# Kernel optimization log

Hardware: AMD Instinct MI355X
Metric: run time of the kernel (lower is better)

The kernel has to match this reference:

```python
import jax, jax.numpy as jnp
import numpy as np

N = 100000      # nodes
E = 1200000     # edges (before self-loops)
DIN = 64        # n_input
DH = 64         # n_hidden
DOUT = 40       # n_output (classes)
L = 2           # n_layers
K = 4           # n_heads
ALPHA = 0.2
EPS = 1e-5


def setup_inputs() -> dict:
    key = jax.random.key(0)
    ks = jax.random.split(key, 12)
    s = lambda k, shape: jax.random.normal(k, shape, jnp.float32) * 0.05
    return {
        "x": jax.random.normal(ks[0], (N, DIN), jnp.float32),
        "edge_index": jax.random.randint(ks[1], (2, E), 0, N),
        # GCNConv weights: per layer l, per head k. conv_h: hidden->hidden, conv_x: input->hidden
        "Wh": s(ks[2], (L, K, DH, DH)), "bh": jnp.zeros((L, K, DH), jnp.float32),
        "Wx": s(ks[3], (L, K, DIN, DH)), "bx": jnp.zeros((L, K, DH), jnp.float32),
        # shared GatedModule
        "gf_w": s(ks[4], (2 * DH, 1)), "gf_b": jnp.zeros((1,), jnp.float32),
        "gu_w": s(ks[5], (2 * DH, 1)), "gu_b": jnp.zeros((1,), jnp.float32),
        # per-block FF
        "ff1_w": s(ks[6], (L, DH, DH)), "ff1_b": jnp.zeros((L, DH), jnp.float32),
        "ff2_w": s(ks[7], (L, DH, DH)), "ff2_b": jnp.zeros((L, DH), jnp.float32),
        # classifier head
        "clf1_w": s(ks[8], (DH, DH)), "clf1_b": jnp.zeros((DH,), jnp.float32),
        "clf2_w": s(ks[9], (DH, DOUT)), "clf2_b": jnp.zeros((DOUT,), jnp.float32),
    }


def _layer_norm(h):
    mu = jnp.mean(h, axis=-1, keepdims=True)
    var = jnp.mean((h - mu) ** 2, axis=-1, keepdims=True)
    return (h - mu) * jax.lax.rsqrt(var + EPS)


def reference(x, edge_index, Wh, bh, Wx, bx, gf_w, gf_b, gu_w, gu_b,
              ff1_w, ff1_b, ff2_w, ff2_b, clf1_w, clf1_b, clf2_w, clf2_b):
    # GCN normalization with self-loops: D^-1/2 (A+I) D^-1/2
    loops = jnp.arange(N)
    src = jnp.concatenate([edge_index[0], loops])  # [E+N]
    dst = jnp.concatenate([edge_index[1], loops])
    deg = jax.ops.segment_sum(jnp.ones_like(src, jnp.float32), dst, num_segments=N)
    dinv = jnp.where(deg > 0, jax.lax.rsqrt(jnp.maximum(deg, 1e-12)), 0.0)
    norm = dinv[src] * dinv[dst]  # [E+N] edge coefficients (shared by all convs)

    def gcn_conv(feat, W, b):
        m = feat @ W                                    # [N, DH] transform first (cheaper)
        agg = jax.ops.segment_sum(m[src] * norm[:, None], dst, num_segments=N)
        return agg + b

    def gate(h, xg):
        g = jnp.concatenate([h, xg], axis=1)            # [N, 2*DH]
        f = ALPHA * jnp.tanh(g @ gf_w + gf_b)
        u = ALPHA * jnp.tanh(g @ gu_w + gu_b)
        return (1.0 + f) * h + (1.0 + u) * xg

    h = jnp.zeros((N, DH), x.dtype)  # h0 = zeros (dropout is identity in eval mode)
    for l in range(L):
        acc = jnp.zeros((N, DH), x.dtype)
        for k in range(K):
            hk = gcn_conv(h, Wh[l, k], bh[l, k])
            xk = gcn_conv(x, Wx[l, k], bx[l, k])
            acc = acc + gate(hk, xk)
        h = acc / K + h                                  # multi-head mean + residual
        h = _layer_norm(h)
        ff = jax.nn.relu(h @ ff1_w[l] + ff1_b[l]) @ ff2_w[l] + ff2_b[l]
        h = _layer_norm(ff + h)
    return jax.nn.relu(h @ clf1_w + clf1_b) @ clf2_w + clf2_b
```

## Files before the change

### kernel.cpp

```cpp
#include <hip/hip_runtime.h>

#define NN 100000
#define EE 1200000
#define ALPHA_C 0.2f
#define EPS_C 1e-5f

typedef __attribute__((ext_vector_type(8))) short short8;
typedef __attribute__((ext_vector_type(4))) float f32x4;
#define MFMA __builtin_amdgcn_mfma_f32_16x16x32_bf16

#define PITCH 72


__device__ __forceinline__ ushort f2bf(float f) {
  unsigned u = __float_as_uint(f);
  unsigned r = (u + 0x7FFFu + ((u >> 16) & 1u)) >> 16;
  return (ushort)r;
}
__device__ __forceinline__ float bf2f(ushort h) { return __uint_as_float((unsigned)h << 16); }

__device__ __forceinline__ float ftanh(float x) {
  float ax = fabsf(x);
  float e = __expf(2.f * ax);
  float t = 1.f - 2.f / (e + 1.f);
  return copysignf(t, x);
}


__global__ __launch_bounds__(256) void k_count(const int* __restrict__ dstv, int* __restrict__ deg) {
  int e = blockIdx.x * 256 + threadIdx.x;
  if (e < EE) atomicAdd(&deg[dstv[e]], 1);
}

__global__ __launch_bounds__(256) void k_scan1(const int* __restrict__ deg, int* __restrict__ rowp,
                                               int* __restrict__ bsum, float* __restrict__ dinv) {
  __shared__ int s[256];
  int t = threadIdx.x;
  int i = blockIdx.x * 256 + t;
  int v = (i < NN) ? deg[i] : 0;
  if (i < NN) dinv[i] = rsqrtf((float)v + 1.0f);
  s[t] = v;
  __syncthreads();
  for (int off = 1; off < 256; off <<= 1) {
    int add = (t >= off) ? s[t - off] : 0;
    __syncthreads();
    s[t] += add;
    __syncthreads();
  }
  if (i < NN) rowp[i] = s[t] - v;
  if (t == 255) bsum[blockIdx.x] = s[255];
}

__global__ __launch_bounds__(512) void k_scan2(int* __restrict__ bsum, int* __restrict__ rowp, int nb) {
  __shared__ int s[512];
  int t = threadIdx.x;
  int v = (t < nb) ? bsum[t] : 0;
  s[t] = v;
  __syncthreads();
  for (int off = 1; off < 512; off <<= 1) {
    int add = (t >= off) ? s[t - off] : 0;
    __syncthreads();
    s[t] += add;
    __syncthreads();
  }
  if (t < nb) bsum[t] = s[t] - v;
  if (t == 0) rowp[NN] = EE;
}

__global__ __launch_bounds__(256) void k_scan3(int* __restrict__ rowp, const int* __restrict__ bsum) {
  int i = blockIdx.x * 256 + threadIdx.x;
  if (i < NN) rowp[i] += bsum[blockIdx.x];
}

__global__ __launch_bounds__(256) void k_fill(const int* __restrict__ srcv, const int* __restrict__ dstv,
                                              const int* __restrict__ rowp, int* __restrict__ fill,
                                              int* __restrict__ col) {
  int e = blockIdx.x * 256 + threadIdx.x;
  if (e < EE) {
    int d = dstv[e];
    int pos = rowp[d] + atomicAdd(&fill[d], 1);
    col[pos] = srcv[e];
  }
}


__global__ __launch_bounds__(256) void k_prescale(const float* __restrict__ feat,
                                                  const float* __restrict__ dinv,
                                                  float* __restrict__ xs) {
  int idx = blockIdx.x * 256 + threadIdx.x;
  if (idx < NN * 16) {
    float4 v = ((const float4*)feat)[idx];
    float d = dinv[idx >> 4];
    v.x *= d; v.y *= d; v.z *= d; v.w *= d;
    ((float4*)xs)[idx] = v;
  }
}

__global__ __launch_bounds__(256) void k_spmm(const float4* __restrict__ xs4, const float* __restrict__ dinv,
                                              const int* __restrict__ rowp, const int* __restrict__ col,
                                              float4* __restrict__ out4) {
  int node = blockIdx.x * 16 + (threadIdx.x >> 4);
  int q = threadIdx.x & 15;
  if (node >= NN) return;
  int s = rowp[node], e = rowp[node + 1];
  float4 a0 = {0.f, 0.f, 0.f, 0.f}, a1 = a0, a2 = a0, a3 = a0;
  int j = s;
  for (; j + 4 <= e; j += 4) {
    int c0 = col[j], c1 = col[j + 1], c2 = col[j + 2], c3 = col[j + 3];
    float4 v0 = xs4[c0 * 16 + q];
    float4 v1 = xs4[c1 * 16 + q];
    float4 v2 = xs4[c2 * 16 + q];
    float4 v3 = xs4[c3 * 16 + q];
    a0 += v0; a1 += v1; a2 += v2; a3 += v3;
  }
  for (; j < e; ++j) a0 += xs4[col[j] * 16 + q];
  float4 sv = xs4[node * 16 + q];
  float d = dinv[node];
  float4 o;
  o.x = d * (a0.x + a1.x + a2.x + a3.x + sv.x);
  o.y = d * (a0.y + a1.y + a2.y + a3.y + sv.y);
  o.z = d * (a0.z + a1.z + a2.z + a3.z + sv.z);
  o.w = d * (a0.w + a1.w + a2.w + a3.w + sv.w);
  out4[node * 16 + q] = o;
}


__global__ __launch_bounds__(256) void k_packz(const float* __restrict__ Wh, const float* __restrict__ Wx,
                                               const float* __restrict__ ff1w, const float* __restrict__ ff2w,
                                               const float* __restrict__ c1w, const float* __restrict__ c2w,
                                               ushort* __restrict__ wpk,
                                               int* __restrict__ deg, int* __restrict__ fill) {
  int i = blockIdx.x * 256 + threadIdx.x;
  if (i < NN) { deg[i] = 0; fill[i] = 0; }
  int id = blockIdx.x;
  if (id >= 22) return;
  const float* src;
  int ncol = 64, vcol = 64;
  if (id < 8) src = Wx + id * 4096;
  else if (id < 16) src = Wh + (id - 8) * 4096;
  else if (id < 18) src = ff1w + (id - 16) * 4096;
  else if (id < 20) src = ff2w + (id - 18) * 4096;
  else if (id == 20) src = c1w;
  else { src = c2w; ncol = 40; vcol = 40; }
  ushort* dst = wpk + (size_t)id * 8192;
  for (int p = threadIdx.x; p < 512; p += 256) {
    int f = p >> 6, l = p & 63;
    int kh = f & 1, tc = f >> 1;
    int r0 = 32 * kh + 8 * (l >> 4), c = 16 * tc + (l & 15);
#pragma unroll
    for (int j = 0; j < 8; ++j) {
      float v = (c < vcol) ? src[(r0 + j) * ncol + c] : 0.f;
      ushort h = f2bf(v);
      dst[f * 512 + l * 8 + j] = h;
      dst[4096 + f * 512 + l * 8 + j] = f2bf(v - bf2f(h));
    }
  }
}


__device__ __forceinline__ float red16(float v) {
  v += __shfl_xor(v, 1);
  v += __shfl_xor(v, 2);
  v += __shfl_xor(v, 4);
  v += __shfl_xor(v, 8);
  return v;
}

__device__ __forceinline__ void stage_tile(const float* __restrict__ src, int gbase,
                                           ushort* __restrict__ hi, ushort* __restrict__ lo, int t) {
#pragma unroll
  for (int u = 0; u < 4; ++u) {
    int f = u * 256 + t;
    int row = f >> 4, c4 = (f & 15) << 2;
    int gr = gbase + row;
    if (gr > NN - 1) gr = NN - 1;
    float4 v = *(const float4*)(src + gr * 64 + c4);
    ushort h0 = f2bf(v.x), h1 = f2bf(v.y), h2 = f2bf(v.z), h3 = f2bf(v.w);
    ushort l0 = f2bf(v.x - bf2f(h0)), l1 = f2bf(v.y - bf2f(h1)),
           l2 = f2bf(v.z - bf2f(h2)), l3 = f2bf(v.w - bf2f(h3));
    int o = row * PITCH + c4;
    *(ushort4*)(hi + o) = make_ushort4(h0, h1, h2, h3);
    *(ushort4*)(lo + o) = make_ushort4(l0, l1, l2, l3);
  }
}

__device__ __forceinline__ void stageB(const ushort* __restrict__ wp, ushort* __restrict__ bsta, int t) {
#pragma unroll
  for (int u = 0; u < 4; ++u) {
    int o = (u * 256 + t) * 8;
    *(short8*)(bsta + o) = *(const short8*)(wp + o);
  }
}

template <int NT>
__device__ __forceinline__ void mm_mfma_l(short8 a0h, short8 a1h, short8 a0l, short8 a1l,
                                          const ushort* __restrict__ bsta, int l, f32x4* C) {
#pragma unroll
  for (int tc = 0; tc < NT; ++tc) {
#pragma unroll
    for (int kh = 0; kh < 2; ++kh) {
      const short8 bh = *(const short8*)(bsta + (tc * 2 + kh) * 512 + l * 8);
      const short8 bl = *(const short8*)(bsta + 4096 + (tc * 2 + kh) * 512 + l * 8);
      const short8 ah = kh ? a1h : a0h;
      const short8 alo = kh ? a1l : a0l;
      C[tc] = MFMA(ah, bh, C[tc], 0, 0, 0);
      C[tc] = MFMA(ah, bl, C[tc], 0, 0, 0);
      C[tc] = MFMA(alo, bh, C[tc], 0, 0, 0);
    }
  }
}

__device__ __forceinline__ void ln_frag(float v[4][4]) {
#pragma unroll
  for (int r = 0; r < 4; ++r) {
    float s = v[0][r] + v[1][r] + v[2][r] + v[3][r];
    s = red16(s);
    float mu = s * 0.015625f;
    float q = 0.f;
#pragma unroll
    for (int tc = 0; tc < 4; ++tc) { float d = v[tc][r] - mu; q = fmaf(d, d, q); }
    q = red16(q);
    float inv = rsqrtf(q * 0.015625f + EPS_C);
#pragma unroll
    for (int tc = 0; tc < 4; ++tc) v[tc][r] = (v[tc][r] - mu) * inv;
  }
}


template <int HAS_H, int WSC, int DO_CLF>
__global__ __launch_bounds__(256) void k_layer(
    const float* __restrict__ aggX, const float* __restrict__ aggH,
    const float* __restrict__ h_in, float* __restrict__ h_out,
    float* __restrict__ hs_out, const float* __restrict__ dinv,
    const ushort* __restrict__ wxp, const ushort* __restrict__ whp,
    const float* __restrict__ bxl, const float* __restrict__ bhl,
    const float* __restrict__ gfw, const float* __restrict__ gfb,
    const float* __restrict__ guw, const float* __restrict__ gub,
    const ushort* __restrict__ ff1p, const float* __restrict__ ff1b,
    const ushort* __restrict__ ff2p, const float* __restrict__ ff2b,
    const ushort* __restrict__ c1p, const float* __restrict__ c1b,
    const ushort* __restrict__ c2p, const float* __restrict__ c2b,
    float* __restrict__ outv) {
  __shared__ __align__(16) ushort th[64 * PITCH], tl[64 * PITCH];
  __shared__ __align__(16) ushort bsta[8192];
  const int t = threadIdx.x, blk = blockIdx.x;
  const int w = t >> 6, l = t & 63, lg = l >> 4, lr = l & 15;
  const int abase = (16 * w + lr) * PITCH + 8 * lg;

  stage_tile(aggX, blk * 64, th, tl, t);
  __syncthreads();
  short8 xa0h = *(const short8*)(th + abase);
  short8 xa1h = *(const short8*)(th + abase + 32);
  short8 xa0l = *(const short8*)(tl + abase);
  short8 xa1l = *(const short8*)(tl + abase + 32);
  short8 ha0h = (short8)0, ha1h = (short8)0, ha0l = (short8)0, ha1l = (short8)0;
  if (HAS_H) {
    __syncthreads();
    stage_tile(aggH, blk * 64, th, tl, t);
    __syncthreads();
    ha0h = *(const short8*)(th + abase);
    ha1h = *(const short8*)(th + abase + 32);
    ha0l = *(const short8*)(tl + abase);
    ha1l = *(const short8*)(tl + abase + 32);
  }

  float gfhw[4], gfxw[4], guhw[4], guxw[4];
#pragma unroll
  for (int tc = 0; tc < 4; ++tc) {
    gfhw[tc] = gfw[lr + 16 * tc]; gfxw[tc] = gfw[64 + lr + 16 * tc];
    guhw[tc] = guw[lr + 16 * tc]; guxw[tc] = guw[64 + lr + 16 * tc];
  }
  const float gfb0 = gfb[0], gub0 = gub[0];

  float acc[4][4];
#pragma unroll
  for (int tc = 0; tc < 4; ++tc)
#pragma unroll
    for (int r = 0; r < 4; ++r) acc[tc][r] = 0.f;

  for (int k = 0; k < 4; ++k) {
    f32x4 cx[4], ch[4];
#pragma unroll
    for (int tc = 0; tc < 4; ++tc) { cx[tc] = (f32x4)0.f; ch[tc] = (f32x4)0.f; }
    __syncthreads();
    stageB(wxp + k * 8192, bsta, t);
    __syncthreads();
    mm_mfma_l<4>(xa0h, xa1h, xa0l, xa1l, bsta, l, cx);
    if (HAS_H) {
      __syncthreads();
      stageB(whp + k * 8192, bsta, t);
      __syncthreads();
      mm_mfma_l<4>(ha0h, ha1h, ha0l, ha1l, bsta, l, ch);
    }

    float Cx[4][4], Ch[4][4];
#pragma unroll
    for (int tc = 0; tc < 4; ++tc) {
      float bxv = bxl[k * 64 + lr + 16 * tc];
      float bhv = bhl[k * 64 + lr + 16 * tc];
#pragma unroll
      for (int r = 0; r < 4; ++r) {
        Cx[tc][r] = cx[tc][r] + bxv;
        Ch[tc][r] = (HAS_H ? ch[tc][r] : 0.f) + bhv;
      }
    }
#pragma unroll
    for (int r = 0; r < 4; ++r) {
      float pf = 0.f, pu = 0.f;
#pragma unroll
      for (int tc = 0; tc < 4; ++tc) {
        pf = fmaf(Ch[tc][r], gfhw[tc], pf); pf = fmaf(Cx[tc][r], gfxw[tc], pf);
        pu = fmaf(Ch[tc][r], guhw[tc], pu); pu = fmaf(Cx[tc][r], guxw[tc], pu);
      }
      pf = red16(pf); pu = red16(pu);
      float fv = ALPHA_C * ftanh(pf + gfb0);
      float uv = ALPHA_C * ftanh(pu + gub0);
#pragma unroll
      for (int tc = 0; tc < 4; ++tc)
        acc[tc][r] += (1.f + fv) * Ch[tc][r] + (1.f + uv) * Cx[tc][r];
    }
  }

  float hmid[4][4];
#pragma unroll
  for (int tc = 0; tc < 4; ++tc)
#pragma unroll
    for (int r = 0; r < 4; ++r) {
      float hv = 0.f;
      if (HAS_H) {
        int gn = blk * 64 + 16 * w + 4 * lg + r;
        if (gn > NN - 1) gn = NN - 1;
        hv = h_in[gn * 64 + lr + 16 * tc];
      }
      hmid[tc][r] = fmaf(acc[tc][r], 0.25f, hv);
    }
  ln_frag(hmid);

  __syncthreads();
#pragma unroll
  for (int tc = 0; tc < 4; ++tc)
#pragma unroll
    for (int r = 0; r < 4; ++r) {
      int o = (16 * w + 4 * lg + r) * PITCH + lr + 16 * tc;
      ushort h = f2bf(hmid[tc][r]);
      th[o] = h;
      tl[o] = f2bf(hmid[tc][r] - bf2f(h));
    }
  __syncthreads();
  short8 m0h = *(const short8*)(th + abase);
  short8 m1h = *(const short8*)(th + abase + 32);
  short8 m0l = *(const short8*)(tl + abase);
  short8 m1l = *(const short8*)(tl + abase + 32);

  f32x4 f1[4];
#pragma unroll
  for (int tc = 0; tc < 4; ++tc) f1[tc] = (f32x4)0.f;
  __syncthreads();
  stageB(ff1p, bsta, t);
  __syncthreads();
  mm_mfma_l<4>(m0h, m1h, m0l, m1l, bsta, l, f1);
#pragma unroll
  for (int tc = 0; tc < 4; ++tc) {
    float bv = ff1b[lr + 16 * tc];
#pragma unroll
    for (int r = 0; r < 4; ++r) {
      float v = fmaxf(f1[tc][r] + bv, 0.f);
      int o = (16 * w + 4 * lg + r) * PITCH + lr + 16 * tc;
      ushort h = f2bf(v);
      th[o] = h;
      tl[o] = f2bf(v - bf2f(h));
    }
  }
  __syncthreads();
  short8 g0h = *(const short8*)(th + abase);
  short8 g1h = *(const short8*)(th + abase + 32);
  short8 g0l = *(const short8*)(tl + abase);
  short8 g1l = *(const short8*)(tl + abase + 32);

  f32x4 f2[4];
#pragma unroll
  for (int tc = 0; tc < 4; ++tc) f2[tc] = (f32x4)0.f;
  __syncthreads();
  stageB(ff2p, bsta, t);
  __syncthreads();
  mm_mfma_l<4>(g0h, g1h, g0l, g1l, bsta, l, f2);
  float F2[4][4];
#pragma unroll
  for (int tc = 0; tc < 4; ++tc) {
    float bv = ff2b[lr + 16 * tc];
#pragma unroll
    for (int r = 0; r < 4; ++r) F2[tc][r] = f2[tc][r] + bv + hmid[tc][r];
  }
  ln_frag(F2);

  if (!DO_CLF) {
#pragma unroll
    for (int r = 0; r < 4; ++r) {
      int gn = blk * 64 + 16 * w + 4 * lg + r;
      if (gn < NN) {
        float dv = WSC ? dinv[gn] : 0.f;
#pragma unroll
        for (int tc = 0; tc < 4; ++tc) {
          h_out[gn * 64 + lr + 16 * tc] = F2[tc][r];
          if (WSC) hs_out[gn * 64 + lr + 16 * tc] = F2[tc][r] * dv;
        }
      }
    }
    return;
  }

  __syncthreads();
#pragma unroll
  for (int tc = 0; tc < 4; ++tc)
#pragma unroll
    for (int r = 0; r < 4; ++r) {
      int o = (16 * w + 4 * lg + r) * PITCH + lr + 16 * tc;
      ushort h = f2bf(F2[tc][r]);
      th[o] = h;
      tl[o] = f2bf(F2[tc][r] - bf2f(h));
    }
  stageB(c1p, bsta, t);
  __syncthreads();
  short8 p0h = *(const short8*)(th + abase);
  short8 p1h = *(const short8*)(th + abase + 32);
  short8 p0l = *(const short8*)(tl + abase);
  short8 p1l = *(const short8*)(tl + abase + 32);

  f32x4 c1[4];
#pragma unroll
  for (int tc = 0; tc < 4; ++tc) c1[tc] = (f32x4)0.f;
  mm_mfma_l<4>(p0h, p1h, p0l, p1l, bsta, l, c1);
  __syncthreads();
#pragma unroll
  for (int tc = 0; tc < 4; ++tc) {
    float bv = c1b[lr + 16 * tc];
#pragma unroll
    for (int r = 0; r < 4; ++r) {
      float v = fmaxf(c1[tc][r] + bv, 0.f);
      int o = (16 * w + 4 * lg + r) * PITCH + lr + 16 * tc;
      ushort hh = f2bf(v);
      th[o] = hh;
      tl[o] = f2bf(v - bf2f(hh));
    }
  }
  stageB(c2p, bsta, t);
  __syncthreads();
  short8 q0h = *(const short8*)(th + abase);
  short8 q1h = *(const short8*)(th + abase + 32);
  short8 q0l = *(const short8*)(tl + abase);
  short8 q1l = *(const short8*)(tl + abase + 32);

  f32x4 c2[3];
#pragma unroll
  for (int tc = 0; tc < 3; ++tc) c2[tc] = (f32x4)0.f;
  mm_mfma_l<3>(q0h, q1h, q0l, q1l, bsta, l, c2);
#pragma unroll
  for (int tc = 0; tc < 3; ++tc) {
    int cc = lr + 16 * tc;
    if (cc < 40) {
      float bv = c2b[cc];
#pragma unroll
      for (int r = 0; r < 4; ++r) {
        int gn = blk * 64 + 16 * w + 4 * lg + r;
        if (gn < NN) outv[gn * 40 + cc] = c2[tc][r] + bv;
      }
    }
  }
}


extern "C" void kernel_launch(void* const* d_in, const int* in_sizes, int n_in,
                              void* d_out, int out_size, void* d_ws, size_t ws_size,
                              hipStream_t stream) {
  (void)in_sizes; (void)n_in; (void)out_size; (void)ws_size;
  const float* x    = (const float*)d_in[0];
  const int*   ei   = (const int*)d_in[1];
  const float* Wh   = (const float*)d_in[2];
  const float* bh   = (const float*)d_in[3];
  const float* Wx   = (const float*)d_in[4];
  const float* bx   = (const float*)d_in[5];
  const float* gfw  = (const float*)d_in[6];
  const float* gfb  = (const float*)d_in[7];
  const float* guw  = (const float*)d_in[8];
  const float* gub  = (const float*)d_in[9];
  const float* ff1w = (const float*)d_in[10];
  const float* ff1b = (const float*)d_in[11];
  const float* ff2w = (const float*)d_in[12];
  const float* ff2b = (const float*)d_in[13];
  const float* c1w  = (const float*)d_in[14];
  const float* c1b  = (const float*)d_in[15];
  const float* c2w  = (const float*)d_in[16];
  const float* c2b  = (const float*)d_in[17];
  float* outv = (float*)d_out;

  char* ws = (char*)d_ws;
  size_t o = 0;
  auto take = [&](size_t b) { char* p = ws + o; o += (b + 255) & ~(size_t)255; return p; };
  int*    deg  = (int*)take((size_t)NN * 4);
  int*    fill = (int*)take((size_t)NN * 4);
  int*    rowp = (int*)take((size_t)(NN + 1) * 4);
  int*    bsum = (int*)take(512 * 4);
  int*    col  = (int*)take((size_t)EE * 4);
  float*  dinv = (float*)take((size_t)NN * 4);
  ushort* wpk  = (ushort*)take((size_t)22 * 8192 * 2);
  float*  aggX = (float*)take((size_t)NN * 64 * 4);
  float*  aggH = (float*)take((size_t)NN * 64 * 4);
  float*  hbuf = (float*)take((size_t)NN * 64 * 4);
  float*  xsc  = (float*)take((size_t)NN * 64 * 4);

  const int* srcv = ei;
  const int* dstv = ei + EE;

  const int NB_E = (EE + 255) / 256;
  const int NB_N = (NN + 255) / 256;
  const int NB_V4 = (NN * 16 + 255) / 256;

  k_packz<<<NB_N, 256, 0, stream>>>(Wh, Wx, ff1w, ff2w, c1w, c2w, wpk, deg, fill);
  k_count<<<NB_E, 256, 0, stream>>>(dstv, deg);
  k_scan1<<<NB_N, 256, 0, stream>>>(deg, rowp, bsum, dinv);
  k_scan2<<<1, 512, 0, stream>>>(bsum, rowp, NB_N);
  k_scan3<<<NB_N, 256, 0, stream>>>(rowp, bsum);
  k_fill<<<NB_E, 256, 0, stream>>>(srcv, dstv, rowp, fill, col);

  k_prescale<<<NB_V4, 256, 0, stream>>>(x, dinv, xsc);
  k_spmm<<<(NN + 15) / 16, 256, 0, stream>>>((const float4*)xsc, dinv, rowp, col, (float4*)aggX);

  const int NB_L = (NN + 63) / 64;
  k_layer<0, 1, 0><<<NB_L, 256, 0, stream>>>(
      aggX, aggX, hbuf, hbuf, xsc, dinv,
      wpk + 0 * 8192, wpk + 8 * 8192, bx, bh, gfw, gfb, guw, gub,
      wpk + 16 * 8192, ff1b, wpk + 18 * 8192, ff2b,
      wpk + 20 * 8192, c1b, wpk + 21 * 8192, c2b, outv);

  k_spmm<<<(NN + 15) / 16, 256, 0, stream>>>((const float4*)xsc, dinv, rowp, col, (float4*)aggH);

  k_layer<1, 0, 1><<<NB_L, 256, 0, stream>>>(
      aggX, aggH, hbuf, hbuf, xsc, dinv,
      wpk + 4 * 8192, wpk + 12 * 8192, bx + 256, bh + 256, gfw, gfb, guw, gub,
      wpk + 17 * 8192, ff1b + 64, wpk + 19 * 8192, ff2b + 64,
      wpk + 20 * 8192, c1b, wpk + 21 * 8192, c2b, outv);
}
```

Measured before the change: 380.9 us.

## Emit bf16 hi/lo split from SpMM and record edge rank during counting

The SpMM kernel now writes its aggregated features directly as packed bf16 hi/lo halves. The layer kernels then load their MFMA A-fragments straight from global memory, with no shared-memory staging, conversion or barriers. Separately, the degree-count kernel stores each edge's atomic rank, so the CSR fill pass no longer needs a second atomic pass or a fill array. The cost is an extra 4.8 MB rank buffer and per-lane strided global loads in place of the LDS tile.

Measured after the change: 338.0 us. 1.13x faster.

```diff
diff --git a/kernel.cpp b/kernel.cpp
--- a/kernel.cpp
+++ b/kernel.cpp
@@ -27,9 +27,10 @@
 }
 
 
-__global__ __launch_bounds__(256) void k_count(const int* __restrict__ dstv, int* __restrict__ deg) {
+__global__ __launch_bounds__(256) void k_countrank(const int* __restrict__ dstv,
+                                                   int* __restrict__ deg, int* __restrict__ rank) {
   int e = blockIdx.x * 256 + threadIdx.x;
-  if (e < EE) atomicAdd(&deg[dstv[e]], 1);
+  if (e < EE) rank[e] = atomicAdd(&deg[dstv[e]], 1);
 }
 
 __global__ __launch_bounds__(256) void k_scan1(const int* __restrict__ deg, int* __restrict__ rowp,
@@ -73,14 +74,10 @@
 }
 
 __global__ __launch_bounds__(256) void k_fill(const int* __restrict__ srcv, const int* __restrict__ dstv,
-                                              const int* __restrict__ rowp, int* __restrict__ fill,
+                                              const int* __restrict__ rowp, const int* __restrict__ rank,
                                               int* __restrict__ col) {
   int e = blockIdx.x * 256 + threadIdx.x;
-  if (e < EE) {
-    int d = dstv[e];
-    int pos = rowp[d] + atomicAdd(&fill[d], 1);
-    col[pos] = srcv[e];
-  }
+  if (e < EE) col[rowp[dstv[e]] + rank[e]] = srcv[e];
 }
 
 
@@ -98,7 +95,7 @@
 
 __global__ __launch_bounds__(256) void k_spmm(const float4* __restrict__ xs4, const float* __restrict__ dinv,
                                               const int* __restrict__ rowp, const int* __restrict__ col,
-                                              float4* __restrict__ out4) {
+                                              ushort* __restrict__ outP) {
   int node = blockIdx.x * 16 + (threadIdx.x >> 4);
   int q = threadIdx.x & 15;
   if (node >= NN) return;
@@ -121,17 +118,21 @@
   o.y = d * (a0.y + a1.y + a2.y + a3.y + sv.y);
   o.z = d * (a0.z + a1.z + a2.z + a3.z + sv.z);
   o.w = d * (a0.w + a1.w + a2.w + a3.w + sv.w);
-  out4[node * 16 + q] = o;
+  ushort h0 = f2bf(o.x), h1 = f2bf(o.y), h2 = f2bf(o.z), h3 = f2bf(o.w);
+  ushort l0 = f2bf(o.x - bf2f(h0)), l1 = f2bf(o.y - bf2f(h1)),
+         l2 = f2bf(o.z - bf2f(h2)), l3 = f2bf(o.w - bf2f(h3));
+  ushort* p = outP + (size_t)node * 128 + 4 * q;
+  *(ushort4*)(p) = make_ushort4(h0, h1, h2, h3);
+  *(ushort4*)(p + 64) = make_ushort4(l0, l1, l2, l3);
 }
 
 
 __global__ __launch_bounds__(256) void k_packz(const float* __restrict__ Wh, const float* __restrict__ Wx,
                                                const float* __restrict__ ff1w, const float* __restrict__ ff2w,
                                                const float* __restrict__ c1w, const float* __restrict__ c2w,
-                                               ushort* __restrict__ wpk,
-                                               int* __restrict__ deg, int* __restrict__ fill) {
+                                               ushort* __restrict__ wpk, int* __restrict__ deg) {
   int i = blockIdx.x * 256 + threadIdx.x;
-  if (i < NN) { deg[i] = 0; fill[i] = 0; }
+  if (i < NN) deg[i] = 0;
   int id = blockIdx.x;
   if (id >= 22) return;
   const float* src;
@@ -166,24 +167,6 @@
   return v;
 }
 
-__device__ __forceinline__ void stage_tile(const float* __restrict__ src, int gbase,
-                                           ushort* __restrict__ hi, ushort* __restrict__ lo, int t) {
-#pragma unroll
-  for (int u = 0; u < 4; ++u) {
-    int f = u * 256 + t;
-    int row = f >> 4, c4 = (f & 15) << 2;
-    int gr = gbase + row;
-    if (gr > NN - 1) gr = NN - 1;
-    float4 v = *(const float4*)(src + gr * 64 + c4);
-    ushort h0 = f2bf(v.x), h1 = f2bf(v.y), h2 = f2bf(v.z), h3 = f2bf(v.w);
-    ushort l0 = f2bf(v.x - bf2f(h0)), l1 = f2bf(v.y - bf2f(h1)),
-           l2 = f2bf(v.z - bf2f(h2)), l3 = f2bf(v.w - bf2f(h3));
-    int o = row * PITCH + c4;
-    *(ushort4*)(hi + o) = make_ushort4(h0, h1, h2, h3);
-    *(ushort4*)(lo + o) = make_ushort4(l0, l1, l2, l3);
-  }
-}
-
 __device__ __forceinline__ void stageB(const ushort* __restrict__ wp, ushort* __restrict__ bsta, int t) {
 #pragma unroll
   for (int u = 0; u < 4; ++u) {
@@ -229,7 +212,7 @@
 
 template <int HAS_H, int WSC, int DO_CLF>
 __global__ __launch_bounds__(256) void k_layer(
-    const float* __restrict__ aggX, const float* __restrict__ aggH,
+    const ushort* __restrict__ aggXP, const ushort* __restrict__ aggHP,
     const float* __restrict__ h_in, float* __restrict__ h_out,
     float* __restrict__ hs_out, const float* __restrict__ dinv,
     const ushort* __restrict__ wxp, const ushort* __restrict__ whp,
@@ -246,22 +229,21 @@
   const int t = threadIdx.x, blk = blockIdx.x;
   const int w = t >> 6, l = t & 63, lg = l >> 4, lr = l & 15;
   const int abase = (16 * w + lr) * PITCH + 8 * lg;
-
-  stage_tile(aggX, blk * 64, th, tl, t);
-  __syncthreads();
-  short8 xa0h = *(const short8*)(th + abase);
-  short8 xa1h = *(const short8*)(th + abase + 32);
-  short8 xa0l = *(const short8*)(tl + abase);
-  short8 xa1l = *(const short8*)(tl + abase + 32);
+  const int arow = blk * 64 + 16 * w + lr;
+  const int arowc = arow < NN ? arow : NN - 1;
+
+  const ushort* axp = aggXP + (size_t)arowc * 128 + 8 * lg;
+  short8 xa0h = *(const short8*)(axp);
+  short8 xa1h = *(const short8*)(axp + 32);
+  short8 xa0l = *(const short8*)(axp + 64);
+  short8 xa1l = *(const short8*)(axp + 96);
   short8 ha0h = (short8)0, ha1h = (short8)0, ha0l = (short8)0, ha1l = (short8)0;
   if (HAS_H) {
-    __syncthreads();
-    stage_tile(aggH, blk * 64, th, tl, t);
-    __syncthreads();
-    ha0h = *(const short8*)(th + abase);
-    ha1h = *(const short8*)(th + abase + 32);
-    ha0l = *(const short8*)(tl + abase);
-    ha1l = *(const short8*)(tl + abase + 32);
+    const ushort* ahp = aggHP + (size_t)arowc * 128 + 8 * lg;
+    ha0h = *(const short8*)(ahp);
+    ha1h = *(const short8*)(ahp + 32);
+    ha0l = *(const short8*)(ahp + 64);
+    ha1l = *(const short8*)(ahp + 96);
   }
 
   float gfhw[4], gfxw[4], guhw[4], guxw[4];
@@ -497,14 +479,14 @@
   size_t o = 0;
   auto take = [&](size_t b) { char* p = ws + o; o += (b + 255) & ~(size_t)255; return p; };
   int*    deg  = (int*)take((size_t)NN * 4);
-  int*    fill = (int*)take((size_t)NN * 4);
+  int*    rank = (int*)take((size_t)EE * 4);
   int*    rowp = (int*)take((size_t)(NN + 1) * 4);
   int*    bsum = (int*)take(512 * 4);
   int*    col  = (int*)take((size_t)EE * 4);
   float*  dinv = (float*)take((size_t)NN * 4);
   ushort* wpk  = (ushort*)take((size_t)22 * 8192 * 2);
-  float*  aggX = (float*)take((size_t)NN * 64 * 4);
-  float*  aggH = (float*)take((size_t)NN * 64 * 4);
+  ushort* aggXP = (ushort*)take((size_t)NN * 128 * 2);
+  ushort* aggHP = (ushort*)take((size_t)NN * 128 * 2);
   float*  hbuf = (float*)take((size_t)NN * 64 * 4);
   float*  xsc  = (float*)take((size_t)NN * 64 * 4);
 
@@ -515,27 +497,27 @@
   const int NB_N = (NN + 255) / 256;
   const int NB_V4 = (NN * 16 + 255) / 256;
 
-  k_packz<<<NB_N, 256, 0, stream>>>(Wh, Wx, ff1w, ff2w, c1w, c2w, wpk, deg, fill);
-  k_count<<<NB_E, 256, 0, stream>>>(dstv, deg);
+  k_packz<<<NB_N, 256, 0, stream>>>(Wh, Wx, ff1w, ff2w, c1w, c2w, wpk, deg);
+  k_countrank<<<NB_E, 256, 0, stream>>>(dstv, deg, rank);
   k_scan1<<<NB_N, 256, 0, stream>>>(deg, rowp, bsum, dinv);
   k_scan2<<<1, 512, 0, stream>>>(bsum, rowp, NB_N);
   k_scan3<<<NB_N, 256, 0, stream>>>(rowp, bsum);
-  k_fill<<<NB_E, 256, 0, stream>>>(srcv, dstv, rowp, fill, col);
+  k_fill<<<NB_E, 256, 0, stream>>>(srcv, dstv, rowp, rank, col);
 
   k_prescale<<<NB_V4, 256, 0, stream>>>(x, dinv, xsc);
-  k_spmm<<<(NN + 15) / 16, 256, 0, stream>>>((const float4*)xsc, dinv, rowp, col, (float4*)aggX);
+  k_spmm<<<(NN + 15) / 16, 256, 0, stream>>>((const float4*)xsc, dinv, rowp, col, aggXP);
 
   const int NB_L = (NN + 63) / 64;
   k_layer<0, 1, 0><<<NB_L, 256, 0, stream>>>(
-      aggX, aggX, hbuf, hbuf, xsc, dinv,
+      aggXP, aggXP, hbuf, hbuf, xsc, dinv,
       wpk + 0 * 8192, wpk + 8 * 8192, bx, bh, gfw, gfb, guw, gub,
       wpk + 16 * 8192, ff1b, wpk + 18 * 8192, ff2b,
       wpk + 20 * 8192, c1b, wpk + 21 * 8192, c2b, outv);
 
-  k_spmm<<<(NN + 15) / 16, 256, 0, stream>>>((const float4*)xsc, dinv, rowp, col, (float4*)aggH);
+  k_spmm<<<(NN + 15) / 16, 256, 0, stream>>>((const float4*)xsc, dinv, rowp, col, aggHP);
 
   k_layer<1, 0, 1><<<NB_L, 256, 0, stream>>>(
-      aggX, aggH, hbuf, hbuf, xsc, dinv,
+      aggXP, aggHP, hbuf, hbuf, xsc, dinv,
       wpk + 4 * 8192, wpk + 12 * 8192, bx + 256, bh + 256, gfw, gfb, guw, gub,
       wpk + 17 * 8192, ff1b + 64, wpk + 19 * 8192, ff2b + 64,
       wpk + 20 * 8192, c1b, wpk + 21 * 8192, c2b, outv);
```
